# Kernel tuning notes

Measured on AMD Instinct MI355X. Metric: run time of the kernel, lower is better.

Reference implementation:

```python
import jax, jax.numpy as jnp
import numpy as np

N_HEADS = 4
HEAD_DIM = 32
N_GROUPS = 32
EPS = 1e-5


def setup_inputs() -> dict:
    key = jax.random.key(0)
    ks = jax.random.split(key, 4)
    B, C, H, W = 2, 128, 64, 64
    x = jax.random.normal(ks[0], (B, C, H, W), dtype=jnp.float32)
    t = jax.random.normal(ks[1], (B,), dtype=jnp.float32)
    norm_w = jnp.ones((C,), dtype=jnp.float32)
    norm_b = jnp.zeros((C,), dtype=jnp.float32)
    proj_w = jax.random.normal(ks[2], (3 * N_HEADS * HEAD_DIM, C), dtype=jnp.float32) * 0.02
    proj_b = jnp.zeros((3 * N_HEADS * HEAD_DIM,), dtype=jnp.float32)
    out_w = jax.random.normal(ks[3], (C, N_HEADS * HEAD_DIM), dtype=jnp.float32) * 0.02
    out_b = jnp.zeros((C,), dtype=jnp.float32)
    return {"x": x, "t": t, "norm_w": norm_w, "norm_b": norm_b,
            "proj_w": proj_w, "proj_b": proj_b, "out_w": out_w, "out_b": out_b}


def reference(x, t, norm_w, norm_b, proj_w, proj_b, out_w, out_b):
    B, C = x.shape[0], x.shape[1]
    Hh, d = N_HEADS, HEAD_DIM
    scale = d ** -0.5
    # GroupNorm over (channels-per-group, spatial)
    xg = x.reshape(B, N_GROUPS, -1)
    mean = jnp.mean(xg, axis=-1, keepdims=True)
    var = jnp.var(xg, axis=-1, keepdims=True)
    xn = ((xg - mean) * jax.lax.rsqrt(var + EPS)).reshape(x.shape)
    xn = xn * norm_w[None, :, None, None] + norm_b[None, :, None, None]
    # tokens: [B, N, C]
    h = xn.reshape(B, C, -1).transpose(0, 2, 1)
    x_tok = x.reshape(B, C, -1).transpose(0, 2, 1)  # residual (pre-norm)
    N = h.shape[1]
    qkv = (h @ proj_w.T + proj_b).reshape(B, N, Hh, 3 * d)
    q, k, v = jnp.split(qkv, 3, axis=-1)  # each [B, N, H, d]
    attn = jnp.einsum('bihd,bjhd->bijh', q, k) * scale  # [B, N, N, H]
    attn = jax.nn.softmax(attn, axis=2)
    out = jnp.einsum('bijh,bjhd->bihd', attn, v).reshape(B, N, Hh * d)
    out = out @ out_w.T + out_b
    return out + x_tok  # [B, N, C]
```

## Files before the change

kernel.cpp:

```cpp
#include <hip/hip_runtime.h>
#include <hip/hip_bf16.h>

typedef __bf16 bf16x8 __attribute__((ext_vector_type(8)));
typedef __bf16 bf16x4 __attribute__((ext_vector_type(4)));
typedef float f32x4 __attribute__((ext_vector_type(4)));

#define QSCALE (0.17677669529663689f * 1.44269504088896340736f)

__device__ __forceinline__ f32x4 mfma_16x16x32(bf16x8 a, bf16x8 b, f32x4 c) {
  return __builtin_amdgcn_mfma_f32_16x16x32_bf16(a, b, c, 0, 0, 0);
}

__global__ __launch_bounds__(256) void gn_stats(const float* __restrict__ x,
                                                float* __restrict__ stats) {
  int bg = blockIdx.x;
  const f32x4* base = (const f32x4*)(x + (size_t)bg * 16384);
  float s = 0.f, ss = 0.f;
  for (int i = threadIdx.x; i < 4096; i += 256) {
    f32x4 v = base[i];
    s += v[0] + v[1] + v[2] + v[3];
    ss += v[0]*v[0] + v[1]*v[1] + v[2]*v[2] + v[3]*v[3];
  }
  #pragma unroll
  for (int off = 32; off; off >>= 1) {
    s += __shfl_down(s, off);
    ss += __shfl_down(ss, off);
  }
  __shared__ float rs[4], rss[4];
  int wid = threadIdx.x >> 6;
  if ((threadIdx.x & 63) == 0) { rs[wid] = s; rss[wid] = ss; }
  __syncthreads();
  if (threadIdx.x == 0) {
    float S = rs[0] + rs[1] + rs[2] + rs[3];
    float SS = rss[0] + rss[1] + rss[2] + rss[3];
    float mean = S * (1.f / 16384.f);
    float var = SS * (1.f / 16384.f) - mean * mean;
    stats[bg * 2] = mean;
    stats[bg * 2 + 1] = rsqrtf(var + 1e-5f);
  }
}

__global__ __launch_bounds__(256) void qkv_kernel(
    const float* __restrict__ x, const float* __restrict__ stats,
    const float* __restrict__ nw, const float* __restrict__ nb,
    const float* __restrict__ pw, const float* __restrict__ pb,
    __bf16* __restrict__ Qb, __bf16* __restrict__ Kb, __bf16* __restrict__ Vb) {
  __shared__ __bf16 ht[16 * 128];
  int chunk = blockIdx.x & 255;
  int b = blockIdx.x >> 8;
  int tid = threadIdx.x;
  int n0 = chunk * 16;
  {
    int tok = tid >> 4, c0 = (tid & 15) * 8;
    float hv[8];
    #pragma unroll
    for (int j = 0; j < 8; ++j) {
      int c = c0 + j;
      float v = x[((size_t)b * 128 + c) * 4096 + n0 + tok];
      float mean = stats[(b * 32 + (c >> 2)) * 2];
      float rstd = stats[(b * 32 + (c >> 2)) * 2 + 1];
      hv[j] = (v - mean) * rstd * nw[c] + nb[c];
    }
    bf16x8 hb;
    #pragma unroll
    for (int j = 0; j < 8; ++j) hb[j] = (__bf16)hv[j];
    int byte = (tok * 256 + c0 * 2) ^ ((tok & 7) << 4);
    *(bf16x8*)((char*)ht + byte) = hb;
  }
  int wave = tid >> 6, lane = tid & 63;
  int g = lane >> 4, r = lane & 15;
  int hh = wave;
  bf16x8 wf[6][4];
  const float* wbase = pw + (size_t)(hh * 96 + r) * 128 + 8 * g;
  #pragma unroll
  for (int ot = 0; ot < 6; ++ot)
    #pragma unroll
    for (int ks = 0; ks < 4; ++ks) {
      const float* p = wbase + ot * 16 * 128 + ks * 32;
      f32x4 a = *(const f32x4*)p;
      f32x4 bq = *(const f32x4*)(p + 4);
      bf16x8 w;
      #pragma unroll
      for (int i = 0; i < 4; ++i) { w[i] = (__bf16)a[i]; w[4 + i] = (__bf16)bq[i]; }
      wf[ot][ks] = w;
    }
  __syncthreads();
  bf16x8 bfr[4];
  #pragma unroll
  for (int ks = 0; ks < 4; ++ks) {
    int byte = (r * 256 + (ks * 32 + 8 * g) * 2) ^ ((r & 7) << 4);
    bfr[ks] = *(const bf16x8*)((char*)ht + byte);
  }
  f32x4 acc[6];
  #pragma unroll
  for (int ot = 0; ot < 6; ++ot) acc[ot] = (f32x4){0.f, 0.f, 0.f, 0.f};
  #pragma unroll
  for (int ks = 0; ks < 4; ++ks)
    #pragma unroll
    for (int ot = 0; ot < 6; ++ot)
      acc[ot] = mfma_16x16x32(wf[ot][ks], bfr[ks], acc[ot]);
  int bh = b * 4 + hh;
  int n = n0 + r;
  #pragma unroll
  for (int ot = 0; ot < 6; ++ot) {
    int o_lo = ot * 16 + 4 * g;
    f32x4 bias = *(const f32x4*)(pb + hh * 96 + o_lo);
    f32x4 v = acc[ot];
    if (ot < 2) {
      bf16x4 qv;
      #pragma unroll
      for (int i = 0; i < 4; ++i) qv[i] = (__bf16)((v[i] + bias[i]) * QSCALE);
      *(bf16x4*)(Qb + ((size_t)bh * 4096 + n) * 32 + o_lo) = qv;
    } else if (ot < 4) {
      bf16x4 kv;
      #pragma unroll
      for (int i = 0; i < 4; ++i) kv[i] = (__bf16)(v[i] + bias[i]);
      *(bf16x4*)(Kb + ((size_t)bh * 4096 + n) * 32 + (o_lo - 32)) = kv;
    } else {
      #pragma unroll
      for (int i = 0; i < 4; ++i) {
        int d = o_lo - 64 + i;
        int jr = n & 31, jb2 = n >> 5;
        int reg = ((jr >> 4) << 2) | (jr & 3);
        int gg = (jr >> 2) & 3;
        int half = d >> 4;
        int lane2 = gg * 16 + (d & 15);
        Vb[(((size_t)bh * 128 + jb2) * 2 + half) * 512 + lane2 * 8 + reg] =
            (__bf16)(v[i] + bias[i]);
      }
    }
  }
}

__global__ __launch_bounds__(256) void attn_kernel(
    const __bf16* __restrict__ Qb, const __bf16* __restrict__ Kb,
    const __bf16* __restrict__ Vb, __bf16* __restrict__ Op,
    float* __restrict__ Lp) {
  int bh = blockIdx.x & 7;
  int rest = blockIdx.x >> 3;
  int ks = rest & 3;
  int qt = rest >> 2;
  int wave = threadIdx.x >> 6;
  int lane = threadIdx.x & 63;
  int g = lane >> 4, r = lane & 15;
  int qi = qt * 128 + wave * 32 + r;
  bf16x8 qf0 = *(const bf16x8*)(Qb + ((size_t)bh * 4096 + qi) * 32 + 8 * g);
  bf16x8 qf1 = *(const bf16x8*)(Qb + ((size_t)bh * 4096 + qi + 16) * 32 + 8 * g);
  const __bf16* kbase = Kb + (size_t)bh * 131072 + r * 32 + 8 * g;
  const bf16x8* vbase = (const bf16x8*)(Vb + (size_t)bh * 131072) + lane;
  bf16x8 ones;
  #pragma unroll
  for (int i = 0; i < 8; ++i) ones[i] = (__bf16)1.0f;
  f32x4 acc00 = {0.f,0.f,0.f,0.f}, acc01 = {0.f,0.f,0.f,0.f};
  f32x4 acc10 = {0.f,0.f,0.f,0.f}, acc11 = {0.f,0.f,0.f,0.f};
  f32x4 accd0 = {0.f,0.f,0.f,0.f}, accd1 = {0.f,0.f,0.f,0.f};
  int jb0 = ks * 32, jbE = jb0 + 32;
  bf16x8 kc0 = *(const bf16x8*)(kbase + jb0 * 1024);
  bf16x8 kc1 = *(const bf16x8*)(kbase + jb0 * 1024 + 512);
  bf16x8 vc0 = vbase[jb0 * 128];
  bf16x8 vc1 = vbase[jb0 * 128 + 64];
  for (int jb = jb0; jb < jbE; ++jb) {
    int jn = (jb + 1 < jbE) ? jb + 1 : jb;
    bf16x8 kn0 = *(const bf16x8*)(kbase + jn * 1024);
    bf16x8 kn1 = *(const bf16x8*)(kbase + jn * 1024 + 512);
    bf16x8 vn0 = vbase[jn * 128];
    bf16x8 vn1 = vbase[jn * 128 + 64];
    f32x4 z = {0.f, 0.f, 0.f, 0.f};
    f32x4 s00 = mfma_16x16x32(kc0, qf0, z);
    f32x4 s01 = mfma_16x16x32(kc1, qf0, z);
    f32x4 s10 = mfma_16x16x32(kc0, qf1, z);
    f32x4 s11 = mfma_16x16x32(kc1, qf1, z);
    float p0[8], p1[8];
    #pragma unroll
    for (int i = 0; i < 4; ++i) {
      p0[i]     = __builtin_amdgcn_exp2f(s00[i]);
      p0[4 + i] = __builtin_amdgcn_exp2f(s01[i]);
      p1[i]     = __builtin_amdgcn_exp2f(s10[i]);
      p1[4 + i] = __builtin_amdgcn_exp2f(s11[i]);
    }
    bf16x8 pf0, pf1;
    #pragma unroll
    for (int i = 0; i < 8; ++i) { pf0[i] = (__bf16)p0[i]; pf1[i] = (__bf16)p1[i]; }
    acc00 = mfma_16x16x32(vc0, pf0, acc00);
    acc01 = mfma_16x16x32(vc1, pf0, acc01);
    acc10 = mfma_16x16x32(vc0, pf1, acc10);
    acc11 = mfma_16x16x32(vc1, pf1, acc11);
    accd0 = mfma_16x16x32(ones, pf0, accd0);
    accd1 = mfma_16x16x32(ones, pf1, accd1);
    kc0 = kn0; kc1 = kn1; vc0 = vn0; vc1 = vn1;
  }
  size_t base = (size_t)(ks * 8 + bh) * 4096 + qi;
  bf16x4 o00, o01, o10, o11;
  #pragma unroll
  for (int i = 0; i < 4; ++i) {
    o00[i] = (__bf16)acc00[i]; o01[i] = (__bf16)acc01[i];
    o10[i] = (__bf16)acc10[i]; o11[i] = (__bf16)acc11[i];
  }
  *(bf16x4*)(Op + base * 32 + 4 * g) = o00;
  *(bf16x4*)(Op + base * 32 + 16 + 4 * g) = o01;
  *(bf16x4*)(Op + (base + 16) * 32 + 4 * g) = o10;
  *(bf16x4*)(Op + (base + 16) * 32 + 16 + 4 * g) = o11;
  if (g == 0) { Lp[base] = accd0[0]; Lp[base + 16] = accd1[0]; }
}

__global__ __launch_bounds__(256) void proj_out_kernel(
    const __bf16* __restrict__ Op, const float* __restrict__ Lp,
    const float* __restrict__ ow, const float* __restrict__ ob,
    const float* __restrict__ x, float* __restrict__ out) {
  __shared__ __bf16 ol[2048];
  __shared__ float rl[16][4];
  int b = blockIdx.x >> 8;
  int n0 = (blockIdx.x & 255) * 16;
  int tid = threadIdx.x;
  if (tid < 64) {
    int t = tid >> 2, hh = tid & 3;
    size_t qidx = (size_t)(b * 4 + hh) * 4096 + n0 + t;
    float l = Lp[qidx] + Lp[qidx + 8 * 4096] + Lp[qidx + 16 * 4096] +
              Lp[qidx + 24 * 4096];
    rl[t][hh] = 1.f / l;
  }
  __syncthreads();
  {
    int t = tid >> 4, p8 = (tid & 15) * 8;
    int hh = p8 >> 5;
    size_t base = ((size_t)(b * 4 + hh) * 4096 + n0 + t) * 32 + (p8 & 31);
    float s[8] = {0.f, 0.f, 0.f, 0.f, 0.f, 0.f, 0.f, 0.f};
    #pragma unroll
    for (int ks = 0; ks < 4; ++ks) {
      bf16x8 v = *(const bf16x8*)(Op + base + (size_t)ks * 1048576);
      #pragma unroll
      for (int j = 0; j < 8; ++j) s[j] += (float)v[j];
    }
    float sc = rl[t][hh];
    bf16x8 ob8;
    #pragma unroll
    for (int j = 0; j < 8; ++j) ob8[j] = (__bf16)(s[j] * sc);
    int byte = (t * 256 + p8 * 2) ^ ((t & 7) << 4);
    *(bf16x8*)((char*)ol + byte) = ob8;
  }
  __syncthreads();
  int wave = tid >> 6, lane = tid & 63;
  int g = lane >> 4, r = lane & 15;
  bf16x8 bfr[4];
  #pragma unroll
  for (int ks = 0; ks < 4; ++ks) {
    int byte = (r * 256 + ks * 64 + g * 16) ^ ((r & 7) << 4);
    bfr[ks] = *(const bf16x8*)((char*)ol + byte);
  }
  f32x4 acc[2];
  #pragma unroll
  for (int ot = 0; ot < 2; ++ot) {
    acc[ot] = (f32x4){0.f, 0.f, 0.f, 0.f};
    const float* wrow = ow + (size_t)(wave * 32 + ot * 16 + r) * 128 + 8 * g;
    #pragma unroll
    for (int ks = 0; ks < 4; ++ks) {
      f32x4 a = *(const f32x4*)(wrow + ks * 32);
      f32x4 bq = *(const f32x4*)(wrow + ks * 32 + 4);
      bf16x8 w;
      #pragma unroll
      for (int i = 0; i < 4; ++i) { w[i] = (__bf16)a[i]; w[4 + i] = (__bf16)bq[i]; }
      acc[ot] = mfma_16x16x32(w, bfr[ks], acc[ot]);
    }
  }
  int n = n0 + r;
  #pragma unroll
  for (int ot = 0; ot < 2; ++ot) {
    int c0 = wave * 32 + ot * 16 + 4 * g;
    f32x4 bias = *(const f32x4*)(ob + c0);
    f32x4 o = acc[ot];
    #pragma unroll
    for (int i = 0; i < 4; ++i)
      o[i] += bias[i] + x[((size_t)b * 128 + c0 + i) * 4096 + n];
    *(f32x4*)(out + ((size_t)b * 4096 + n) * 128 + c0) = o;
  }
}

extern "C" void kernel_launch(void* const* d_in, const int* in_sizes, int n_in,
                              void* d_out, int out_size, void* d_ws, size_t ws_size,
                              hipStream_t stream) {
  const float* x  = (const float*)d_in[0];
  const float* nw = (const float*)d_in[2];
  const float* nb = (const float*)d_in[3];
  const float* pw = (const float*)d_in[4];
  const float* pb = (const float*)d_in[5];
  const float* ow = (const float*)d_in[6];
  const float* ob = (const float*)d_in[7];
  float* out = (float*)d_out;

  char* ws = (char*)d_ws;
  float* stats = (float*)ws;
  __bf16* Qb = (__bf16*)(ws + 1024);
  __bf16* Kb = (__bf16*)(ws + 1024 + 2097152);
  __bf16* Vb = (__bf16*)(ws + 1024 + 4194304);
  __bf16* Op = (__bf16*)(ws + 1024 + 6291456);
  float*  Lp = (float*)(ws + 1024 + 14680064);

  gn_stats<<<64, 256, 0, stream>>>(x, stats);
  qkv_kernel<<<512, 256, 0, stream>>>(x, stats, nw, nb, pw, pb, Qb, Kb, Vb);
  attn_kernel<<<1024, 256, 0, stream>>>(Qb, Kb, Vb, Op, Lp);
  proj_out_kernel<<<512, 256, 0, stream>>>(Op, Lp, ow, ob, x, out);
}
```

Before: 132.4 us.

## Stage K/V tiles via LDS with async loads, pre-pack bf16 weights, coalesce residual

Adds a prep kernel that converts projection weights to bf16 in MFMA fragment order, so qkv and output-projection kernels load packed fragments instead of converting fp32 per block. K is written in a fragment-packed layout, and the attention kernel stages each K/V tile once per block into double-buffered LDS with global_load_lds, in place of every wave loading it from global. The output kernel stages the residual x through shared memory with vectorized loads instead of strided scalar reads. The trade-offs are an extra launch and a per-iteration __syncthreads in the attention loop.

```diff
diff --git a/kernel.cpp b/kernel.cpp
--- a/kernel.cpp
+++ b/kernel.cpp
@@ -9,6 +9,36 @@
 
 __device__ __forceinline__ f32x4 mfma_16x16x32(bf16x8 a, bf16x8 b, f32x4 c) {
   return __builtin_amdgcn_mfma_f32_16x16x32_bf16(a, b, c, 0, 0, 0);
+}
+
+__global__ __launch_bounds__(256) void prep_weights(
+    const float* __restrict__ pw, const float* __restrict__ ow,
+    __bf16* __restrict__ Wp, __bf16* __restrict__ Wq) {
+  int idx = blockIdx.x * 256 + threadIdx.x;
+  const float* src;
+  __bf16* dst;
+  if (idx < 6144) {
+    int lane = idx & 63, ks = (idx >> 6) & 3;
+    int rest = idx >> 8;
+    int ot = rest % 6, hh = rest / 6;
+    src = pw + (size_t)(hh * 96 + ot * 16 + (lane & 15)) * 128 + ks * 32 +
+          8 * (lane >> 4);
+    dst = Wp + (size_t)idx * 8;
+  } else {
+    int j = idx - 6144;
+    int lane = j & 63, ks = (j >> 6) & 3;
+    int rest = j >> 8;
+    int ot = rest & 1, wv = rest >> 1;
+    src = ow + (size_t)(wv * 32 + ot * 16 + (lane & 15)) * 128 + ks * 32 +
+          8 * (lane >> 4);
+    dst = Wq + (size_t)j * 8;
+  }
+  f32x4 a = *(const f32x4*)src;
+  f32x4 b2 = *(const f32x4*)(src + 4);
+  bf16x8 w;
+  #pragma unroll
+  for (int i = 0; i < 4; ++i) { w[i] = (__bf16)a[i]; w[4 + i] = (__bf16)b2[i]; }
+  *(bf16x8*)dst = w;
 }
 
 __global__ __launch_bounds__(256) void gn_stats(const float* __restrict__ x,
@@ -43,8 +73,8 @@
 __global__ __launch_bounds__(256) void qkv_kernel(
     const float* __restrict__ x, const float* __restrict__ stats,
     const float* __restrict__ nw, const float* __restrict__ nb,
-    const float* __restrict__ pw, const float* __restrict__ pb,
-    __bf16* __restrict__ Qb, __bf16* __restrict__ Kb, __bf16* __restrict__ Vb) {
+    const __bf16* __restrict__ Wp, const float* __restrict__ pb,
+    __bf16* __restrict__ Qb, __bf16* __restrict__ Kp, __bf16* __restrict__ Vb) {
   __shared__ __bf16 ht[16 * 128];
   int chunk = blockIdx.x & 255;
   int b = blockIdx.x >> 8;
@@ -71,19 +101,12 @@
   int g = lane >> 4, r = lane & 15;
   int hh = wave;
   bf16x8 wf[6][4];
-  const float* wbase = pw + (size_t)(hh * 96 + r) * 128 + 8 * g;
+  const bf16x8* wpp = (const bf16x8*)Wp;
   #pragma unroll
   for (int ot = 0; ot < 6; ++ot)
     #pragma unroll
-    for (int ks = 0; ks < 4; ++ks) {
-      const float* p = wbase + ot * 16 * 128 + ks * 32;
-      f32x4 a = *(const f32x4*)p;
-      f32x4 bq = *(const f32x4*)(p + 4);
-      bf16x8 w;
-      #pragma unroll
-      for (int i = 0; i < 4; ++i) { w[i] = (__bf16)a[i]; w[4 + i] = (__bf16)bq[i]; }
-      wf[ot][ks] = w;
-    }
+    for (int ks = 0; ks < 4; ++ks)
+      wf[ot][ks] = wpp[((hh * 6 + ot) * 4 + ks) * 64 + lane];
   __syncthreads();
   bf16x8 bfr[4];
   #pragma unroll
@@ -115,7 +138,11 @@
       bf16x4 kv;
       #pragma unroll
       for (int i = 0; i < 4; ++i) kv[i] = (__bf16)(v[i] + bias[i]);
-      *(bf16x4*)(Kb + ((size_t)bh * 4096 + n) * 32 + (o_lo - 32)) = kv;
+      size_t koff = ((size_t)(bh * 128 + (n >> 5))) * 1024 +
+                    (size_t)((n >> 4) & 1) * 512 +
+                    ((n & 15) + 16 * ((ot - 2) * 2 + (g >> 1))) * 8 +
+                    (g & 1) * 4;
+      *(bf16x4*)(Kp + koff) = kv;
     } else {
       #pragma unroll
       for (int i = 0; i < 4; ++i) {
@@ -133,9 +160,11 @@
 }
 
 __global__ __launch_bounds__(256) void attn_kernel(
-    const __bf16* __restrict__ Qb, const __bf16* __restrict__ Kb,
+    const __bf16* __restrict__ Qb, const __bf16* __restrict__ Kp,
     const __bf16* __restrict__ Vb, __bf16* __restrict__ Op,
     float* __restrict__ Lp) {
+  __shared__ __bf16 kls[2][1024];
+  __shared__ __bf16 vls[2][1024];
   int bh = blockIdx.x & 7;
   int rest = blockIdx.x >> 3;
   int ks = rest & 3;
@@ -146,25 +175,38 @@
   int qi = qt * 128 + wave * 32 + r;
   bf16x8 qf0 = *(const bf16x8*)(Qb + ((size_t)bh * 4096 + qi) * 32 + 8 * g);
   bf16x8 qf1 = *(const bf16x8*)(Qb + ((size_t)bh * 4096 + qi + 16) * 32 + 8 * g);
-  const __bf16* kbase = Kb + (size_t)bh * 131072 + r * 32 + 8 * g;
-  const bf16x8* vbase = (const bf16x8*)(Vb + (size_t)bh * 131072) + lane;
+  const __bf16* ktile = Kp + (size_t)bh * 131072;
+  const __bf16* vtile = Vb + (size_t)bh * 131072;
   bf16x8 ones;
   #pragma unroll
   for (int i = 0; i < 8; ++i) ones[i] = (__bf16)1.0f;
   f32x4 acc00 = {0.f,0.f,0.f,0.f}, acc01 = {0.f,0.f,0.f,0.f};
   f32x4 acc10 = {0.f,0.f,0.f,0.f}, acc11 = {0.f,0.f,0.f,0.f};
   f32x4 accd0 = {0.f,0.f,0.f,0.f}, accd1 = {0.f,0.f,0.f,0.f};
-  int jb0 = ks * 32, jbE = jb0 + 32;
-  bf16x8 kc0 = *(const bf16x8*)(kbase + jb0 * 1024);
-  bf16x8 kc1 = *(const bf16x8*)(kbase + jb0 * 1024 + 512);
-  bf16x8 vc0 = vbase[jb0 * 128];
-  bf16x8 vc1 = vbase[jb0 * 128 + 64];
-  for (int jb = jb0; jb < jbE; ++jb) {
-    int jn = (jb + 1 < jbE) ? jb + 1 : jb;
-    bf16x8 kn0 = *(const bf16x8*)(kbase + jn * 1024);
-    bf16x8 kn1 = *(const bf16x8*)(kbase + jn * 1024 + 512);
-    bf16x8 vn0 = vbase[jn * 128];
-    bf16x8 vn1 = vbase[jn * 128 + 64];
+  int jb0 = ks * 32;
+  auto stage = [&](int buf, int jb) {
+    const __bf16* src;
+    __bf16* dst;
+    if (wave < 2) {
+      src = ktile + jb * 1024 + wave * 512 + lane * 8;
+      dst = &kls[buf][wave * 512];
+    } else {
+      src = vtile + jb * 1024 + (wave - 2) * 512 + lane * 8;
+      dst = &vls[buf][(wave - 2) * 512];
+    }
+    __builtin_amdgcn_global_load_lds(
+        (const __attribute__((address_space(1))) uint32_t*)src,
+        (__attribute__((address_space(3))) uint32_t*)dst, 16, 0, 0);
+  };
+  stage(0, jb0);
+  __syncthreads();
+  for (int t = 0; t < 32; ++t) {
+    int buf = t & 1;
+    if (t + 1 < 32) stage(buf ^ 1, jb0 + t + 1);
+    bf16x8 kc0 = *(const bf16x8*)&kls[buf][lane * 8];
+    bf16x8 kc1 = *(const bf16x8*)&kls[buf][512 + lane * 8];
+    bf16x8 vc0 = *(const bf16x8*)&vls[buf][lane * 8];
+    bf16x8 vc1 = *(const bf16x8*)&vls[buf][512 + lane * 8];
     f32x4 z = {0.f, 0.f, 0.f, 0.f};
     f32x4 s00 = mfma_16x16x32(kc0, qf0, z);
     f32x4 s01 = mfma_16x16x32(kc1, qf0, z);
@@ -187,7 +229,7 @@
     acc11 = mfma_16x16x32(vc1, pf1, acc11);
     accd0 = mfma_16x16x32(ones, pf0, accd0);
     accd1 = mfma_16x16x32(ones, pf1, accd1);
-    kc0 = kn0; kc1 = kn1; vc0 = vn0; vc1 = vn1;
+    __syncthreads();
   }
   size_t base = (size_t)(ks * 8 + bh) * 4096 + qi;
   bf16x4 o00, o01, o10, o11;
@@ -205,10 +247,11 @@
 
 __global__ __launch_bounds__(256) void proj_out_kernel(
     const __bf16* __restrict__ Op, const float* __restrict__ Lp,
-    const float* __restrict__ ow, const float* __restrict__ ob,
+    const __bf16* __restrict__ Wq, const float* __restrict__ ob,
     const float* __restrict__ x, float* __restrict__ out) {
   __shared__ __bf16 ol[2048];
   __shared__ float rl[16][4];
+  __shared__ float xl[128][20];
   int b = blockIdx.x >> 8;
   int n0 = (blockIdx.x & 255) * 16;
   int tid = threadIdx.x;
@@ -219,6 +262,14 @@
               Lp[qidx + 24 * 4096];
     rl[t][hh] = 1.f / l;
   }
+  {
+    int c = tid >> 1, hf = tid & 1;
+    const float* xs = x + ((size_t)b * 128 + c) * 4096 + n0 + hf * 8;
+    f32x4 x0 = *(const f32x4*)xs;
+    f32x4 x1 = *(const f32x4*)(xs + 4);
+    *(f32x4*)&xl[c][hf * 8] = x0;
+    *(f32x4*)&xl[c][hf * 8 + 4] = x1;
+  }
   __syncthreads();
   {
     int t = tid >> 4, p8 = (tid & 15) * 8;
@@ -247,20 +298,15 @@
     int byte = (r * 256 + ks * 64 + g * 16) ^ ((r & 7) << 4);
     bfr[ks] = *(const bf16x8*)((char*)ol + byte);
   }
+  const bf16x8* wqp = (const bf16x8*)Wq;
   f32x4 acc[2];
   #pragma unroll
   for (int ot = 0; ot < 2; ++ot) {
     acc[ot] = (f32x4){0.f, 0.f, 0.f, 0.f};
-    const float* wrow = ow + (size_t)(wave * 32 + ot * 16 + r) * 128 + 8 * g;
-    #pragma unroll
-    for (int ks = 0; ks < 4; ++ks) {
-      f32x4 a = *(const f32x4*)(wrow + ks * 32);
-      f32x4 bq = *(const f32x4*)(wrow + ks * 32 + 4);
-      bf16x8 w;
-      #pragma unroll
-      for (int i = 0; i < 4; ++i) { w[i] = (__bf16)a[i]; w[4 + i] = (__bf16)bq[i]; }
-      acc[ot] = mfma_16x16x32(w, bfr[ks], acc[ot]);
-    }
+    #pragma unroll
+    for (int ks = 0; ks < 4; ++ks)
+      acc[ot] = mfma_16x16x32(wqp[((wave * 2 + ot) * 4 + ks) * 64 + lane],
+                              bfr[ks], acc[ot]);
   }
   int n = n0 + r;
   #pragma unroll
@@ -269,8 +315,7 @@
     f32x4 bias = *(const f32x4*)(ob + c0);
     f32x4 o = acc[ot];
     #pragma unroll
-    for (int i = 0; i < 4; ++i)
-      o[i] += bias[i] + x[((size_t)b * 128 + c0 + i) * 4096 + n];
+    for (int i = 0; i < 4; ++i) o[i] += bias[i] + xl[c0 + i][r];
     *(f32x4*)(out + ((size_t)b * 4096 + n) * 128 + c0) = o;
   }
 }
@@ -290,13 +335,16 @@
   char* ws = (char*)d_ws;
   float* stats = (float*)ws;
   __bf16* Qb = (__bf16*)(ws + 1024);
-  __bf16* Kb = (__bf16*)(ws + 1024 + 2097152);
+  __bf16* Kp = (__bf16*)(ws + 1024 + 2097152);
   __bf16* Vb = (__bf16*)(ws + 1024 + 4194304);
   __bf16* Op = (__bf16*)(ws + 1024 + 6291456);
   float*  Lp = (float*)(ws + 1024 + 14680064);
-
+  __bf16* Wp = (__bf16*)(ws + 1024 + 15204352);
+  __bf16* Wq = (__bf16*)(ws + 1024 + 15302656);
+
+  prep_weights<<<32, 256, 0, stream>>>(pw, ow, Wp, Wq);
   gn_stats<<<64, 256, 0, stream>>>(x, stats);
-  qkv_kernel<<<512, 256, 0, stream>>>(x, stats, nw, nb, pw, pb, Qb, Kb, Vb);
-  attn_kernel<<<1024, 256, 0, stream>>>(Qb, Kb, Vb, Op, Lp);
-  proj_out_kernel<<<512, 256, 0, stream>>>(Op, Lp, ow, ob, x, out);
-}
+  qkv_kernel<<<512, 256, 0, stream>>>(x, stats, nw, nb, Wp, pb, Qb, Kp, Vb);
+  attn_kernel<<<1024, 256, 0, stream>>>(Qb, Kp, Vb, Op, Lp);
+  proj_out_kernel<<<512, 256, 0, stream>>>(Op, Lp, Wq, ob, x, out);
+}
```

Result: faster. 122.0 us (-7.9%).
